# Kernel tuning notes

Measured on AMD Instinct MI355X. Metric: run time of the kernel, lower is better.

## Reference

```python
import jax, jax.numpy as jnp
import numpy as np

T, N, I, H, OUT = 16, 4096, 4, 32, 1


def setup_inputs() -> dict:
    key = jax.random.key(0)
    ks = jax.random.split(key, 12)
    f32 = jnp.float32
    x_path = jax.random.normal(ks[0], (T, N, I), f32)
    adj = jax.random.normal(ks[1], (N, N), f32) / np.float32(np.sqrt(N))
    W_enc = jax.random.normal(ks[2], (I, H), f32) / np.float32(np.sqrt(I))
    b_enc = jnp.zeros((H,), f32)
    W_gcn = jax.random.normal(ks[3], (H, H), f32) / np.float32(np.sqrt(H))
    b_gcn = jnp.zeros((H,), f32)
    W_time = jax.random.normal(ks[4], (H, H), f32) / np.float32(np.sqrt(H))
    b_time = jnp.zeros((H,), f32)
    W_proj = jax.random.normal(ks[5], (H, H * I), f32) * np.float32(0.1 / np.sqrt(H))
    b_proj = jnp.zeros((H * I,), f32)
    W_d1 = jax.random.normal(ks[6], (H, 16), f32) / np.float32(np.sqrt(H))
    b_d1 = jnp.zeros((16,), f32)
    W_d2 = jax.random.normal(ks[7], (16, OUT), f32) / np.float32(4.0)
    b_d2 = jnp.zeros((OUT,), f32)
    return dict(x_path=x_path, adj=adj, W_enc=W_enc, b_enc=b_enc,
                W_gcn=W_gcn, b_gcn=b_gcn, W_time=W_time, b_time=b_time,
                W_proj=W_proj, b_proj=b_proj, W_d1=W_d1, b_d1=b_d1,
                W_d2=W_d2, b_d2=b_d2)


def _natural_cubic_coeffs(y):
    # y: (T, C) samples on uniform grid t=0..T-1 (h=1).
    # Natural cubic spline: tridiagonal solve for second derivatives M.
    Tn = y.shape[0]
    main = jnp.ones((Tn,), y.dtype).at[1:-1].set(4.0)
    A = jnp.diag(main)
    idx = jnp.arange(1, Tn - 1)
    A = A.at[idx, idx - 1].set(1.0).at[idx, idx + 1].set(1.0)
    rhs = jnp.zeros_like(y).at[1:-1].set(6.0 * (y[2:] - 2.0 * y[1:-1] + y[:-2]))
    M = jnp.linalg.solve(A, rhs)
    b = (y[1:] - y[:-1]) - (2.0 * M[:-1] + M[1:]) / 6.0
    c = M[:-1] / 2.0
    d = (M[1:] - M[:-1]) / 6.0
    return b, c, d  # each (T-1, C); dX/dt on interval i at local s: b+2cs+3ds^2


def reference(x_path, adj, W_enc, b_enc, W_gcn, b_gcn, W_time, b_time,
              W_proj, b_proj, W_d1, b_d1, W_d2, b_d2):
    Tn, Nn, In = x_path.shape
    Hn = W_enc.shape[1]
    y = x_path.reshape(Tn, Nn * In)
    sb, sc, sd = _natural_cubic_coeffs(y)

    # z0 = encoder(X(t0)); spline value at grid point 0 equals the sample.
    z0 = x_path[0] @ W_enc + b_enc  # (N, H)

    def vf(z, dxdt):
        # SpatialVectorField + projector + block-diagonal Jacobian applied to dX/dt.
        # z: (N, H), dxdt: (N, I)
        zn = adj @ z                                     # GCN neighbor aggregation
        h = jax.nn.relu(zn @ W_gcn + b_gcn + z @ W_time + b_time)
        sens = (h @ W_proj + b_proj).reshape(Nn, Hn, In)  # per-site Jacobian blocks
        # site_identity * sens -> block-diag; matmul with dX reduces to per-site contraction
        return jnp.einsum('nhi,ni->nh', sens, dxdt)

    def rk4_step(z, coefs):
        bi, ci, di = coefs  # (N*I,)
        def dxdt(s):
            return (bi + 2.0 * ci * s + 3.0 * di * s * s).reshape(Nn, In)
        k1 = vf(z, dxdt(0.0))
        k2 = vf(z + 0.5 * k1, dxdt(0.5))
        k3 = vf(z + 0.5 * k2, dxdt(0.5))
        k4 = vf(z + k3, dxdt(1.0))
        zn = z + (k1 + 2.0 * k2 + 2.0 * k3 + k4) / 6.0
        return zn, zn

    _, zs = jax.lax.scan(rk4_step, z0, (sb, sc, sd))
    zT = jnp.concatenate([z0[None], zs], axis=0)  # (T, N, H)

    hdec = jax.nn.relu(zT @ W_d1 + b_d1)
    return jax.nn.sigmoid(hdec @ W_d2 + b_d2)  # (T, N, OUT)
```

## Files before the change

### kernel.cpp

```cpp
#include <hip/hip_runtime.h>
#include <hip/hip_bf16.h>

#define NN 4096
#define NI 16384
#define HH 32
#define ZLEN (HH * NN)

typedef __attribute__((ext_vector_type(8))) short short8;
typedef __attribute__((ext_vector_type(4))) float f32x4;

__device__ __forceinline__ short f2bs(float f) {
  __hip_bfloat16 b = __float2bfloat16(f);
  return *(short*)&b;
}

__global__ __launch_bounds__(512) void k_cvt(const float* __restrict__ a,
                                             short* __restrict__ ab) {
  const int tid = threadIdx.x;
  const int W = tid >> 6, lane = tid & 63;
  const int fr = lane & 15, oct = lane >> 4;
  const int R = blockIdx.x;
  const float* srow = a + (long)(R * 16 + fr) * NN + W * 512 + oct * 8;
  short* drow = ab + ((long)(R * 8 + W) * 16) * 512 + lane * 8;
#pragma unroll 4
  for (int i = 0; i < 16; ++i) {
    const float4 u0 = *(const float4*)(srow + i * 32);
    const float4 u1 = *(const float4*)(srow + i * 32 + 4);
    short8 r;
    r[0] = f2bs(u0.x); r[1] = f2bs(u0.y); r[2] = f2bs(u0.z); r[3] = f2bs(u0.w);
    r[4] = f2bs(u1.x); r[5] = f2bs(u1.y); r[6] = f2bs(u1.z); r[7] = f2bs(u1.w);
    *(short8*)(drow + i * 512) = r;
  }
}

__device__ __forceinline__ long zt_idx(int n, int h) {
  const int hb = h >> 4, hl = h & 15;
  const int kb = n >> 5, oct = (n >> 3) & 3, j = n & 7;
  return ((long)(hb * 128 + kb) * 64 + hl + 16 * oct) * 8 + j;
}

__global__ void k_spline(const float* __restrict__ x,
                         float* __restrict__ dx0, float* __restrict__ dxh,
                         float* __restrict__ dx1, unsigned* __restrict__ bar) {
  if (blockIdx.x == 0)
    for (int i = threadIdx.x; i < 16384; i += 256) bar[i] = 0u;
  const int c = blockIdx.x * 256 + threadIdx.x;
  float y[16];
#pragma unroll
  for (int t = 0; t < 16; ++t) y[t] = x[t * NI + c];
  float cp[15], dp[15], M[16];
  cp[1] = 0.25f;
  dp[1] = (6.f * (y[2] - 2.f * y[1] + y[0])) * 0.25f;
#pragma unroll
  for (int i = 2; i <= 14; ++i) {
    float ri = 6.f * (y[i + 1] - 2.f * y[i] + y[i - 1]);
    float inv = 1.f / (4.f - cp[i - 1]);
    cp[i] = inv;
    dp[i] = (ri - dp[i - 1]) * inv;
  }
  M[0] = 0.f; M[15] = 0.f;
  M[14] = dp[14];
#pragma unroll
  for (int i = 13; i >= 1; --i) M[i] = dp[i] - cp[i] * M[i + 1];
#pragma unroll
  for (int i = 0; i < 15; ++i) {
    float b = (y[i + 1] - y[i]) - (2.f * M[i] + M[i + 1]) * (1.f / 6.f);
    float cc = 0.5f * M[i];
    float dd = (M[i + 1] - M[i]) * (1.f / 6.f);
    dx0[i * NI + c] = b;
    dxh[i * NI + c] = b + cc + 0.75f * dd;
    dx1[i * NI + c] = b + 2.f * cc + 3.f * dd;
  }
}

struct OdeP {
  const float *x, *We, *be;
  const short *adjb;
  const float *Wg, *bg, *Wt, *bt, *Wp, *bp, *Wd1, *bd1, *Wd2, *bd2;
  const float *dx0, *dxh, *dx1;
  short *ztr;
  unsigned *bar;
  float *out;
};

__device__ __forceinline__ void gbar2(const OdeP& p, int s, int bid, int tid) {
  __syncthreads();
  if (tid == 0) {
    unsigned* stri = p.bar + s * 128;
    unsigned* flg = p.bar + 8192 + s * 16;
    __hip_atomic_fetch_add(&stri[(bid & 7) * 16], 1u,
                           __ATOMIC_RELAXED, __HIP_MEMORY_SCOPE_AGENT);
    if (bid == 0) {
#pragma unroll 1
      for (int x2 = 0; x2 < 8; ++x2)
        while (__hip_atomic_load(&stri[x2 * 16], __ATOMIC_RELAXED,
                                 __HIP_MEMORY_SCOPE_AGENT) < 32u)
          __builtin_amdgcn_s_sleep(2);
      __hip_atomic_store(flg, 1u, __ATOMIC_RELAXED, __HIP_MEMORY_SCOPE_AGENT);
    } else {
      while (__hip_atomic_load(flg, __ATOMIC_RELAXED,
                               __HIP_MEMORY_SCOPE_AGENT) == 0u)
        __builtin_amdgcn_s_sleep(2);
    }
  }
  __syncthreads();
}

__global__ __launch_bounds__(1024) void k_ode(OdeP p) {
  __shared__ float red2[16][32][17];
  __shared__ float zn_s[16][33];
  __shared__ float h_s[16][33];
  __shared__ float ze_s[16][33];
  __shared__ float znt[16][33];
  __shared__ float Wg_s[32][32];
  __shared__ float Wt_s[32][32];
  __shared__ float Wp_s[32][136];
  __shared__ float Wd1_s[32][16];
  __shared__ float bgt_s[32];
  __shared__ float bp_s[128];
  __shared__ float dsm[33];

  const int tid = threadIdx.x;
  const int lane = tid & 63;
  const int w = tid >> 6;
  const int bid = blockIdx.x;
  const int r0 = bid * 16;
  const int lane8 = lane * 8;
  const int r = (tid >> 5) & 15, c = tid & 31;

  if (tid < 1024) {
    Wg_s[tid >> 5][tid & 31] = p.Wg[tid];
    Wt_s[tid >> 5][tid & 31] = p.Wt[tid];
  }
  for (int idx = tid; idx < 4096; idx += 1024)
    Wp_s[idx >> 7][idx & 127] = p.Wp[idx];
  if (tid < 512) Wd1_s[tid >> 4][tid & 15] = p.Wd1[tid];
  if (tid < 32) bgt_s[tid] = p.bg[tid] + p.bt[tid];
  if (tid < 128) bp_s[tid] = p.bp[tid];
  if (tid < 16) { dsm[tid] = p.bd1[tid]; dsm[16 + tid] = p.Wd2[tid]; }
  if (tid == 0) dsm[32] = p.bd2[0];

  float zb = 0.f, k1r = 0.f, k2r = 0.f, k3r = 0.f;
  if (tid < 512) {
    const int n = r0 + r;
    const float4 xv = *(const float4*)&p.x[n * 4];
    float z0 = p.be[c];
    z0 = fmaf(xv.x, p.We[c], z0);
    z0 = fmaf(xv.y, p.We[32 + c], z0);
    z0 = fmaf(xv.z, p.We[64 + c], z0);
    z0 = fmaf(xv.w, p.We[96 + c], z0);
    zb = z0;
    ze_s[r][c] = z0;
    znt[r][c] = z0;
  }
  __syncthreads();

  if (tid < 256) {
    const int rp = tid >> 5, cc = tid & 31, rr = rp * 2;
    const unsigned lo = (unsigned short)f2bs(znt[rr][cc]);
    const unsigned hi = (unsigned short)f2bs(znt[rr + 1][cc]);
    unsigned* dst = (unsigned*)p.ztr + (zt_idx(r0 + rr, cc) >> 1);
    __hip_atomic_store(dst, lo | (hi << 16), __ATOMIC_RELAXED, __HIP_MEMORY_SCOPE_AGENT);
  }
  if (tid < 16) {
    float acc = dsm[32];
#pragma unroll
    for (int jj = 0; jj < 16; ++jj) {
      float hv = dsm[jj];
#pragma unroll
      for (int hh = 0; hh < 32; ++hh) hv = fmaf(znt[tid][hh], Wd1_s[hh][jj], hv);
      acc = fmaf(fmaxf(hv, 0.f), dsm[16 + jj], acc);
    }
    p.out[r0 + tid] = 1.f / (1.f + expf(-acc));
  }
  gbar2(p, 0, bid, tid);

#pragma unroll 1
  for (int s = 0; s < 60; ++s) {
    const int t = s >> 2;
    const int j = (s & 3) + 1;
    const short* zi = p.ztr + (long)s * ZLEN;
    short* zo = p.ztr + (long)(s + 1) * ZLEN;
    const float* dxp = (j == 1) ? (p.dx0 + t * NI)
                     : (j == 4) ? (p.dx1 + t * NI) : (p.dxh + t * NI);

    f32x4 a0 = {0.f, 0.f, 0.f, 0.f}, a1 = {0.f, 0.f, 0.f, 0.f};
    const short* ap  = p.adjb + ((long)(bid * 128 + w * 8)) * 512 + lane8;
    const short* b0p = zi + ((long)(w * 8)) * 512 + lane8;
    const short* b1p = zi + ((long)(128 + w * 8)) * 512 + lane8;
#pragma unroll
    for (int i = 0; i < 8; ++i) {
      const short8 av = *(const short8*)(ap + i * 512);
      const short8 b0 = *(const short8*)(b0p + i * 512);
      const short8 b1 = *(const short8*)(b1p + i * 512);
      a0 = __builtin_amdgcn_mfma_f32_16x16x32_bf16(av, b0, a0, 0, 0, 0);
      a1 = __builtin_amdgcn_mfma_f32_16x16x32_bf16(av, b1, a1, 0, 0, 0);
    }
    {
      const int crow = (lane >> 4) * 4;
      const int ccol = lane & 15;
#pragma unroll
      for (int q = 0; q < 4; ++q) {
        red2[crow + q][ccol][w] = a0[q];
        red2[crow + q][ccol + 16][w] = a1[q];
      }
    }
    __syncthreads();

    if (tid < 512) {
      float zn = 0.f;
#pragma unroll
      for (int q = 0; q < 16; ++q) zn += red2[r][c][q];
      zn_s[r][c] = zn;
    }
    __syncthreads();

    if (tid < 512) {
      float hv = bgt_s[c];
#pragma unroll
      for (int kk = 0; kk < 32; ++kk)
        hv = fmaf(zn_s[r][kk], Wg_s[kk][c], fmaf(ze_s[r][kk], Wt_s[kk][c], hv));
      h_s[r][c] = fmaxf(hv, 0.f);
    }
    __syncthreads();

    if (tid < 512) {
      const int row = r0 + r;
      float hr[32];
#pragma unroll
      for (int hp = 0; hp < 32; ++hp) hr[hp] = h_s[r][hp];
      float s0 = bp_s[c * 4], s1 = bp_s[c * 4 + 1];
      float s2 = bp_s[c * 4 + 2], s3 = bp_s[c * 4 + 3];
#pragma unroll
      for (int hp = 0; hp < 32; ++hp) {
        const float4 wv = *(const float4*)&Wp_s[hp][c * 4];
        s0 = fmaf(hr[hp], wv.x, s0);
        s1 = fmaf(hr[hp], wv.y, s1);
        s2 = fmaf(hr[hp], wv.z, s2);
        s3 = fmaf(hr[hp], wv.w, s3);
      }
      const float4 dxv = *(const float4*)&dxp[row * 4];
      const float kv = s0 * dxv.x + s1 * dxv.y + s2 * dxv.z + s3 * dxv.w;
      float znew;
      if (j == 4) {
        znew = zb + (k1r + 2.f * k2r + 2.f * k3r + kv) * (1.f / 6.f);
        zb = znew;
      } else {
        if (j == 1) k1r = kv; else if (j == 2) k2r = kv; else k3r = kv;
        znew = zb + ((j == 3) ? 1.f : 0.5f) * kv;
      }
      ze_s[r][c] = znew;
      znt[r][c] = znew;
    }
    __syncthreads();

    if (tid < 256) {
      const int rp = tid >> 5, cc = tid & 31, rr = rp * 2;
      const unsigned lo = (unsigned short)f2bs(znt[rr][cc]);
      const unsigned hi = (unsigned short)f2bs(znt[rr + 1][cc]);
      unsigned* dst = (unsigned*)zo + (zt_idx(r0 + rr, cc) >> 1);
      __hip_atomic_store(dst, lo | (hi << 16), __ATOMIC_RELAXED, __HIP_MEMORY_SCOPE_AGENT);
    }

    if (j == 4 && tid < 16) {
      float acc = dsm[32];
#pragma unroll
      for (int jj = 0; jj < 16; ++jj) {
        float hv = dsm[jj];
#pragma unroll
        for (int hh = 0; hh < 32; ++hh) hv = fmaf(znt[tid][hh], Wd1_s[hh][jj], hv);
        acc = fmaf(fmaxf(hv, 0.f), dsm[16 + jj], acc);
      }
      p.out[(t + 1) * NN + r0 + tid] = 1.f / (1.f + expf(-acc));
    }

    if (s < 59) gbar2(p, s + 1, bid, tid);
  }
}

extern "C" void kernel_launch(void* const* d_in, const int* in_sizes, int n_in,
                              void* d_out, int out_size, void* d_ws, size_t ws_size,
                              hipStream_t stream) {
  (void)in_sizes; (void)n_in; (void)out_size; (void)ws_size;
  const float* x      = (const float*)d_in[0];
  const float* adj    = (const float*)d_in[1];
  const float* W_enc  = (const float*)d_in[2];
  const float* b_enc  = (const float*)d_in[3];
  const float* W_gcn  = (const float*)d_in[4];
  const float* b_gcn  = (const float*)d_in[5];
  const float* W_time = (const float*)d_in[6];
  const float* b_time = (const float*)d_in[7];
  const float* W_proj = (const float*)d_in[8];
  const float* b_proj = (const float*)d_in[9];
  const float* W_d1   = (const float*)d_in[10];
  const float* b_d1   = (const float*)d_in[11];
  const float* W_d2   = (const float*)d_in[12];
  const float* b_d2   = (const float*)d_in[13];

  unsigned* bar = (unsigned*)d_ws;
  float* dx0 = (float*)(bar + 16384);
  float* dxh = dx0 + 15 * NI;
  float* dx1 = dxh + 15 * NI;
  short* ztr = (short*)(dx1 + 15 * NI);
  short* adjb = ztr + 61L * ZLEN;

  k_cvt<<<256, 512, 0, stream>>>(adj, adjb);
  k_spline<<<64, 256, 0, stream>>>(x, dx0, dxh, dx1, bar);

  OdeP p;
  p.x = x; p.We = W_enc; p.be = b_enc; p.adjb = adjb;
  p.Wg = W_gcn; p.bg = b_gcn; p.Wt = W_time; p.bt = b_time;
  p.Wp = W_proj; p.bp = b_proj; p.Wd1 = W_d1; p.bd1 = b_d1;
  p.Wd2 = W_d2; p.bd2 = b_d2;
  p.dx0 = dx0; p.dxh = dxh; p.dx1 = dx1;
  p.ztr = ztr; p.bar = bar; p.out = (float*)d_out;

  void* args[] = { &p };
  hipError_t rc = hipLaunchCooperativeKernel((const void*)k_ode, dim3(256), dim3(1024),
                                             args, 0, stream);
  if (rc != hipSuccess) {
    k_ode<<<256, 1024, 0, stream>>>(p);
  }
}
```

Before: 883.8 us.

## Keep block's bf16 adjacency slice resident in LDS and shrink blocks to 512 threads

Drops the separate adjacency conversion kernel. Each persistent block now converts its own 16-row adj slice to bf16 once and keeps it in LDS (128KB), so the 60 ODE stages no longer re-read adjacency from global memory. Blocks shrink to 512 threads, each wave covering twice the K range, and the cross-wave reduction uses LDS atomicAdd instead of a staging buffer plus an extra barrier. W_proj is also held in bf16 in LDS. The trade-offs are much higher LDS use, fewer waves to hide latency, atomic contention on the reduction, and bf16 rounding of W_proj.

Result: slower. 933.9 us (+5.7%).

```diff
diff --git a/kernel.cpp b/kernel.cpp
--- a/kernel.cpp
+++ b/kernel.cpp
@@ -7,30 +7,16 @@
 #define ZLEN (HH * NN)
 
 typedef __attribute__((ext_vector_type(8))) short short8;
+typedef __attribute__((ext_vector_type(4))) short short4v;
 typedef __attribute__((ext_vector_type(4))) float f32x4;
 
 __device__ __forceinline__ short f2bs(float f) {
   __hip_bfloat16 b = __float2bfloat16(f);
   return *(short*)&b;
 }
-
-__global__ __launch_bounds__(512) void k_cvt(const float* __restrict__ a,
-                                             short* __restrict__ ab) {
-  const int tid = threadIdx.x;
-  const int W = tid >> 6, lane = tid & 63;
-  const int fr = lane & 15, oct = lane >> 4;
-  const int R = blockIdx.x;
-  const float* srow = a + (long)(R * 16 + fr) * NN + W * 512 + oct * 8;
-  short* drow = ab + ((long)(R * 8 + W) * 16) * 512 + lane * 8;
-#pragma unroll 4
-  for (int i = 0; i < 16; ++i) {
-    const float4 u0 = *(const float4*)(srow + i * 32);
-    const float4 u1 = *(const float4*)(srow + i * 32 + 4);
-    short8 r;
-    r[0] = f2bs(u0.x); r[1] = f2bs(u0.y); r[2] = f2bs(u0.z); r[3] = f2bs(u0.w);
-    r[4] = f2bs(u1.x); r[5] = f2bs(u1.y); r[6] = f2bs(u1.z); r[7] = f2bs(u1.w);
-    *(short8*)(drow + i * 512) = r;
-  }
+__device__ __forceinline__ float bs2f(short s) {
+  __hip_bfloat16 b = *(__hip_bfloat16*)&s;
+  return __bfloat162float(b);
 }
 
 __device__ __forceinline__ long zt_idx(int n, int h) {
@@ -74,8 +60,7 @@
 }
 
 struct OdeP {
-  const float *x, *We, *be;
-  const short *adjb;
+  const float *x, *We, *be, *adj;
   const float *Wg, *bg, *Wt, *bt, *Wp, *bp, *Wd1, *bd1, *Wd2, *bd2;
   const float *dx0, *dxh, *dx1;
   short *ztr;
@@ -106,15 +91,15 @@
   __syncthreads();
 }
 
-__global__ __launch_bounds__(1024) void k_ode(OdeP p) {
-  __shared__ float red2[16][32][17];
+__global__ __launch_bounds__(512) void k_ode(OdeP p) {
+  __shared__ __align__(16) short adjs[65536];
   __shared__ float zn_s[16][33];
+  __shared__ float ze_s[16][33];
   __shared__ float h_s[16][33];
-  __shared__ float ze_s[16][33];
   __shared__ float znt[16][33];
   __shared__ float Wg_s[32][32];
   __shared__ float Wt_s[32][32];
-  __shared__ float Wp_s[32][136];
+  __shared__ short Wp_s[32][136];
   __shared__ float Wd1_s[32][16];
   __shared__ float bgt_s[32];
   __shared__ float bp_s[128];
@@ -126,22 +111,36 @@
   const int bid = blockIdx.x;
   const int r0 = bid * 16;
   const int lane8 = lane * 8;
-  const int r = (tid >> 5) & 15, c = tid & 31;
-
-  if (tid < 1024) {
-    Wg_s[tid >> 5][tid & 31] = p.Wg[tid];
-    Wt_s[tid >> 5][tid & 31] = p.Wt[tid];
-  }
-  for (int idx = tid; idx < 4096; idx += 1024)
-    Wp_s[idx >> 7][idx & 127] = p.Wp[idx];
+  const int fr = lane & 15, oct = lane >> 4;
+  const int r = tid >> 5, c = tid & 31;
+
+  for (int idx = tid; idx < 1024; idx += 512) {
+    Wg_s[idx >> 5][idx & 31] = p.Wg[idx];
+    Wt_s[idx >> 5][idx & 31] = p.Wt[idx];
+  }
+  for (int idx = tid; idx < 4096; idx += 512)
+    Wp_s[idx >> 7][idx & 127] = f2bs(p.Wp[idx]);
   if (tid < 512) Wd1_s[tid >> 4][tid & 15] = p.Wd1[tid];
   if (tid < 32) bgt_s[tid] = p.bg[tid] + p.bt[tid];
   if (tid < 128) bp_s[tid] = p.bp[tid];
   if (tid < 16) { dsm[tid] = p.bd1[tid]; dsm[16 + tid] = p.Wd2[tid]; }
   if (tid == 0) dsm[32] = p.bd2[0];
 
+  {
+    const float* srow = p.adj + (long)(r0 + fr) * NN + w * 512 + oct * 8;
+#pragma unroll 4
+    for (int i = 0; i < 16; ++i) {
+      const float4 u0 = *(const float4*)(srow + i * 32);
+      const float4 u1 = *(const float4*)(srow + i * 32 + 4);
+      short8 v;
+      v[0] = f2bs(u0.x); v[1] = f2bs(u0.y); v[2] = f2bs(u0.z); v[3] = f2bs(u0.w);
+      v[4] = f2bs(u1.x); v[5] = f2bs(u1.y); v[6] = f2bs(u1.z); v[7] = f2bs(u1.w);
+      *(short8*)&adjs[(w * 16 + i) * 512 + lane8] = v;
+    }
+  }
+
   float zb = 0.f, k1r = 0.f, k2r = 0.f, k3r = 0.f;
-  if (tid < 512) {
+  {
     const int n = r0 + r;
     const float4 xv = *(const float4*)&p.x[n * 4];
     float z0 = p.be[c];
@@ -152,6 +151,7 @@
     zb = z0;
     ze_s[r][c] = z0;
     znt[r][c] = z0;
+    zn_s[r][c] = 0.f;
   }
   __syncthreads();
 
@@ -185,12 +185,12 @@
                      : (j == 4) ? (p.dx1 + t * NI) : (p.dxh + t * NI);
 
     f32x4 a0 = {0.f, 0.f, 0.f, 0.f}, a1 = {0.f, 0.f, 0.f, 0.f};
-    const short* ap  = p.adjb + ((long)(bid * 128 + w * 8)) * 512 + lane8;
-    const short* b0p = zi + ((long)(w * 8)) * 512 + lane8;
-    const short* b1p = zi + ((long)(128 + w * 8)) * 512 + lane8;
-#pragma unroll
-    for (int i = 0; i < 8; ++i) {
-      const short8 av = *(const short8*)(ap + i * 512);
+    const int fb = w * 16;
+    const short* b0p = zi + ((long)fb) * 512 + lane8;
+    const short* b1p = zi + ((long)(128 + fb)) * 512 + lane8;
+#pragma unroll
+    for (int i = 0; i < 16; ++i) {
+      const short8 av = *(const short8*)&adjs[(fb + i) * 512 + lane8];
       const short8 b0 = *(const short8*)(b0p + i * 512);
       const short8 b1 = *(const short8*)(b1p + i * 512);
       a0 = __builtin_amdgcn_mfma_f32_16x16x32_bf16(av, b0, a0, 0, 0, 0);
@@ -201,21 +201,13 @@
       const int ccol = lane & 15;
 #pragma unroll
       for (int q = 0; q < 4; ++q) {
-        red2[crow + q][ccol][w] = a0[q];
-        red2[crow + q][ccol + 16][w] = a1[q];
+        atomicAdd(&zn_s[crow + q][ccol], a0[q]);
+        atomicAdd(&zn_s[crow + q][ccol + 16], a1[q]);
       }
     }
     __syncthreads();
 
-    if (tid < 512) {
-      float zn = 0.f;
-#pragma unroll
-      for (int q = 0; q < 16; ++q) zn += red2[r][c][q];
-      zn_s[r][c] = zn;
-    }
-    __syncthreads();
-
-    if (tid < 512) {
+    {
       float hv = bgt_s[c];
 #pragma unroll
       for (int kk = 0; kk < 32; ++kk)
@@ -224,7 +216,7 @@
     }
     __syncthreads();
 
-    if (tid < 512) {
+    {
       const int row = r0 + r;
       float hr[32];
 #pragma unroll
@@ -233,11 +225,11 @@
       float s2 = bp_s[c * 4 + 2], s3 = bp_s[c * 4 + 3];
 #pragma unroll
       for (int hp = 0; hp < 32; ++hp) {
-        const float4 wv = *(const float4*)&Wp_s[hp][c * 4];
-        s0 = fmaf(hr[hp], wv.x, s0);
-        s1 = fmaf(hr[hp], wv.y, s1);
-        s2 = fmaf(hr[hp], wv.z, s2);
-        s3 = fmaf(hr[hp], wv.w, s3);
+        const short4v wv = *(const short4v*)&Wp_s[hp][c * 4];
+        s0 = fmaf(hr[hp], bs2f(wv[0]), s0);
+        s1 = fmaf(hr[hp], bs2f(wv[1]), s1);
+        s2 = fmaf(hr[hp], bs2f(wv[2]), s2);
+        s3 = fmaf(hr[hp], bs2f(wv[3]), s3);
       }
       const float4 dxv = *(const float4*)&dxp[row * 4];
       const float kv = s0 * dxv.x + s1 * dxv.y + s2 * dxv.z + s3 * dxv.w;
@@ -251,6 +243,7 @@
       }
       ze_s[r][c] = znew;
       znt[r][c] = znew;
+      zn_s[r][c] = 0.f;
     }
     __syncthreads();
 
@@ -302,13 +295,11 @@
   float* dxh = dx0 + 15 * NI;
   float* dx1 = dxh + 15 * NI;
   short* ztr = (short*)(dx1 + 15 * NI);
-  short* adjb = ztr + 61L * ZLEN;
-
-  k_cvt<<<256, 512, 0, stream>>>(adj, adjb);
+
   k_spline<<<64, 256, 0, stream>>>(x, dx0, dxh, dx1, bar);
 
   OdeP p;
-  p.x = x; p.We = W_enc; p.be = b_enc; p.adjb = adjb;
+  p.x = x; p.We = W_enc; p.be = b_enc; p.adj = adj;
   p.Wg = W_gcn; p.bg = b_gcn; p.Wt = W_time; p.bt = b_time;
   p.Wp = W_proj; p.bp = b_proj; p.Wd1 = W_d1; p.bd1 = b_d1;
   p.Wd2 = W_d2; p.bd2 = b_d2;
@@ -316,9 +307,9 @@
   p.ztr = ztr; p.bar = bar; p.out = (float*)d_out;
 
   void* args[] = { &p };
-  hipError_t rc = hipLaunchCooperativeKernel((const void*)k_ode, dim3(256), dim3(1024),
+  hipError_t rc = hipLaunchCooperativeKernel((const void*)k_ode, dim3(256), dim3(512),
                                              args, 0, stream);
   if (rc != hipSuccess) {
-    k_ode<<<256, 1024, 0, stream>>>(p);
-  }
-}
+    k_ode<<<256, 512, 0, stream>>>(p);
+  }
+}
```
